# Kernel optimization log

Measured on AMD Instinct MI355X. Metric: run time of the kernel, lower is better.

The kernel has to match this reference:

```python
import jax, jax.numpy as jnp
import numpy as np

B, CIN, COUT, H, W, K, LATENT = 16, 512, 512, 64, 64, 3, 512
SQRT2 = float(np.sqrt(2.0))


def setup_inputs() -> dict:
    key = jax.random.key(0)
    ks = jax.random.split(key, 6)
    return {
        "x": jax.random.normal(ks[0], (B, CIN, H, W), jnp.float32),
        "latent": jax.random.normal(ks[1], (B, LATENT), jnp.float32),
        "noise": jax.random.normal(ks[2], (B, 1, H, W), jnp.float32),
        "affine_weight": jax.random.normal(ks[3], (CIN, LATENT), jnp.float32),
        "affine_bias": jnp.ones((CIN,), jnp.float32),
        "conv_weight": jax.random.normal(ks[4], (COUT, CIN, K, K), jnp.float32),
        "noise_weight": jax.random.normal(ks[5], (), jnp.float32),
        "bias": jnp.zeros((1, COUT, 1, 1), jnp.float32),
    }


def reference(x, latent, noise, affine_weight, affine_bias, conv_weight, noise_weight, bias):
    # NoiseInjection (applied before conv, as in the source)
    x = x + noise_weight * noise

    # AffineNetwork / EqualLinear: w * sqrt(1/in), leaky_relu(.,0.2)*sqrt(2)
    wmul = 1.0 / jnp.sqrt(jnp.float32(affine_weight.shape[1]))
    style = latent @ (affine_weight * wmul).T + affine_bias[None, :]
    style = jax.nn.leaky_relu(style, 0.2) * SQRT2  # [B, Cin]

    # Per-sample modulation (source overwrites the fan-in multiplier; raw weight used)
    w = conv_weight[None] * style[:, None, :, None, None]  # [B, Cout, Cin, kh, kw]
    demod = jax.lax.rsqrt(jnp.sum(w * w, axis=(2, 3, 4), keepdims=True) + 1e-8)
    w = w * demod

    def conv1(xi, wi):  # xi: [Cin,H,W], wi: [Cout,Cin,kh,kw]
        return jax.lax.conv_general_dilated(
            xi[None], wi, (1, 1), "SAME",
            dimension_numbers=("NCHW", "OIHW", "NCHW"))[0]

    out = jax.vmap(conv1)(x, w)  # [B, Cout, H, W]
    return jax.nn.leaky_relu(out + bias, 0.2) * SQRT2
```

## Files before the change

### kernel.cpp

```cpp
#include <hip/hip_runtime.h>

#define SQRT2F 1.41421356237309515f

typedef __attribute__((ext_vector_type(8))) short short8;
typedef __attribute__((ext_vector_type(4))) float floatx4;

static __device__ __forceinline__ unsigned short f2bf(float f) {
    unsigned int u = __float_as_uint(f);
    u += 0x7fffu + ((u >> 16) & 1u);
    return (unsigned short)(u >> 16);
}

static __device__ __forceinline__ void gl_lds16(const void* g, void* l) {
    __builtin_amdgcn_global_load_lds(
        (const __attribute__((address_space(1))) unsigned int*)g,
        (__attribute__((address_space(3))) unsigned int*)l, 16, 0, 0);
}

__global__ void style_kernel(const float* __restrict__ latent,
                             const float* __restrict__ aw,
                             const float* __restrict__ abias,
                             float* __restrict__ style) {
    const int b = blockIdx.x;
    const int t = threadIdx.x;
    __shared__ float lat[512];
    lat[t]       = latent[b * 512 + t];
    lat[t + 256] = latent[b * 512 + t + 256];
    __syncthreads();
    const float wmul = 0.04419417382415922f;
    for (int c = t; c < 512; c += 256) {
        const float* row = aw + (size_t)c * 512;
        float s = 0.f;
        #pragma unroll 8
        for (int k = 0; k < 512; ++k) s += lat[k] * row[k];
        s = s * wmul + abias[c];
        s = (s > 0.f ? s : 0.2f * s) * SQRT2F;
        style[b * 512 + c] = s;
    }
}

__global__ void wprep_kernel(const float* __restrict__ cw,
                             const float* __restrict__ style,
                             unsigned short* __restrict__ wbf,
                             float* __restrict__ demod) {
    const int co = blockIdx.x;
    const int t = threadIdx.x;
    __shared__ float raw[4608];
    __shared__ float sty2[8192];
    __shared__ float r2[512];
    const float* row = cw + (size_t)co * 4608;
    for (int i = t; i < 4608; i += 256) raw[i] = row[i];
    for (int i = t; i < 8192; i += 256) { float v = style[i]; sty2[i] = v * v; }
    __syncthreads();
    for (int cin = t; cin < 512; cin += 256) {
        float s = 0.f;
        #pragma unroll
        for (int tap = 0; tap < 9; ++tap) { float v = raw[cin * 9 + tap]; s += v * v; }
        r2[cin] = s;
    }
    for (int i = t; i < 4608; i += 256) {
        int cin = i / 9, tap = i - cin * 9;
        wbf[(((size_t)(cin >> 5) * 9 + tap) * 512 + co) * 32 + (cin & 31)] = f2bf(raw[i]);
    }
    __syncthreads();
    const int lane = t & 63, wv = t >> 6;
    #pragma unroll
    for (int bb = 0; bb < 4; ++bb) {
        int b = wv * 4 + bb;
        float s = 0.f;
        for (int cin = lane; cin < 512; cin += 64) s += r2[cin] * sty2[b * 512 + cin];
        #pragma unroll
        for (int off = 32; off > 0; off >>= 1) s += __shfl_down(s, off, 64);
        if (lane == 0) demod[b * 512 + co] = rsqrtf(s + 1e-8f);
    }
}

__global__ void xprep_kernel(const float* __restrict__ x,
                             const float* __restrict__ noise,
                             const float* __restrict__ nwp,
                             const float* __restrict__ style,
                             unsigned short* __restrict__ xp) {
    const int h = blockIdx.x, slab = blockIdx.y, b = blockIdx.z;
    const int t = threadIdx.x;
    __shared__ float tile[32][65];
    const int ci4 = t >> 6, w = t & 63;
    const float nv = nwp[0] * noise[(size_t)b * 4096 + h * 64 + w];
    #pragma unroll
    for (int p = 0; p < 8; ++p) {
        int cl = p * 4 + ci4;
        int cin = slab * 32 + cl;
        float v = x[((size_t)(b * 512 + cin)) * 4096 + h * 64 + w];
        tile[cl][w] = (v + nv) * style[b * 512 + cin];
    }
    __syncthreads();
    const int w2 = t >> 2, chunk = t & 3;
    short8 o;
    #pragma unroll
    for (int j = 0; j < 8; ++j) o[j] = (short)f2bf(tile[chunk * 8 + j][w2]);
    *(short8*)(xp + ((size_t)(b * 16 + slab) * 4356 + (h + 1) * 66 + (w2 + 1)) * 32 + chunk * 8) = o;
}

__launch_bounds__(256, 2)
__global__ void conv_kernel(const unsigned short* __restrict__ xp,
                            const unsigned short* __restrict__ wbf,
                            const float* __restrict__ demod,
                            const float* __restrict__ bias,
                            float* __restrict__ out) {
    const int b   = blockIdx.z;
    const int co0 = blockIdx.y * 128;
    const int tr  = blockIdx.x >> 2, tc = blockIdx.x & 3;
    const int h0  = tr * 8, w0 = tc * 16;
    const int tid  = threadIdx.x;
    const int lane = tid & 63, wv = tid >> 6;
    const int wr = wv >> 1, wc = wv & 1;
    const int quad = lane >> 4, l16 = lane & 15;

    __shared__ __align__(16) unsigned short lds_x[2][6144];
    __shared__ __align__(16) unsigned short lds_w[2][12288];

    floatx4 acc[4][4] = {};

    int wso[6];
    #pragma unroll
    for (int it = 0; it < 6; ++it) {
        int co = (it * 64 + (tid >> 2)) & 127;
        int lchunk = (tid & 3) ^ ((co >> 1) & 3);
        wso[it] = (it >> 1) * 32768 + co * 64 + lchunk * 16;
    }
    int xo[3];
    #pragma unroll
    for (int it = 0; it < 3; ++it) {
        int pos = it * 64 + (tid >> 2);
        if (pos > 179) pos = 179;
        int r = pos / 18, c = pos - r * 18;
        int lchunk = (tid & 3) ^ ((pos >> 1) & 3);
        xo[it] = (r * 66 + c) * 64 + lchunk * 16;
    }
    const int wvb = wv * 1024;

    int a_off[4];
    #pragma unroll
    for (int mi = 0; mi < 4; ++mi) {
        int co = wr * 64 + mi * 16 + l16;
        a_off[mi] = co * 32 + (quad ^ ((co >> 1) & 3)) * 8;
    }
    int bo[4][9];
    #pragma unroll
    for (int ni = 0; ni < 4; ++ni)
        #pragma unroll
        for (int kh = 0; kh < 3; ++kh)
            #pragma unroll
            for (int kw = 0; kw < 3; ++kw) {
                int pos = (wc * 4 + ni + kh) * 18 + kw + l16;
                bo[ni][kh * 3 + kw] = pos * 32 + (quad ^ ((pos >> 1) & 3)) * 8;
            }

    const char* xpb = (const char*)xp + ((size_t)b * 16 * 4356 + h0 * 66 + w0) * 64;
    const char* wb0 = (const char*)wbf + (size_t)co0 * 64;

    #pragma unroll
    for (int it = 0; it < 3; ++it)
        gl_lds16(xpb + xo[it], (char*)lds_x[0] + it * 4096 + wvb);
    #pragma unroll
    for (int it = 0; it < 6; ++it)
        gl_lds16(wb0 + wso[it], (char*)lds_w[0] + it * 4096 + wvb);

    for (int s = 0; s < 16; ++s) {
        #pragma unroll
        for (int g = 0; g < 3; ++g) {
            __syncthreads();
            if (g < 2) {
                const char* gw = wb0 + s * 294912 + (g + 1) * 98304;
                char* lw = (char*)lds_w[(s + g + 1) & 1];
                #pragma unroll
                for (int it = 0; it < 6; ++it)
                    gl_lds16(gw + wso[it], lw + it * 4096 + wvb);
            } else if (s < 15) {
                const char* gw = wb0 + (s + 1) * 294912;
                char* lw = (char*)lds_w[(s + 1) & 1];
                #pragma unroll
                for (int it = 0; it < 6; ++it)
                    gl_lds16(gw + wso[it], lw + it * 4096 + wvb);
            }
            if (g == 0 && s < 15) {
                const char* gx = xpb + (size_t)(s + 1) * 278784;
                char* lx = (char*)lds_x[(s + 1) & 1];
                #pragma unroll
                for (int it = 0; it < 3; ++it)
                    gl_lds16(gx + xo[it], lx + it * 4096 + wvb);
            }
            const unsigned short* wbuf = lds_w[(s + g) & 1];
            const unsigned short* xbuf = lds_x[s & 1];
            #pragma unroll
            for (int tl = 0; tl < 3; ++tl) {
                const int tap = g * 3 + tl;
                short8 a[4], bb[4];
                #pragma unroll
                for (int mi = 0; mi < 4; ++mi)
                    a[mi] = *(const short8*)(wbuf + tl * 4096 + a_off[mi]);
                #pragma unroll
                for (int ni = 0; ni < 4; ++ni)
                    bb[ni] = *(const short8*)(xbuf + bo[ni][tap]);
                #pragma unroll
                for (int mi = 0; mi < 4; ++mi)
                    #pragma unroll
                    for (int ni = 0; ni < 4; ++ni)
                        acc[mi][ni] = __builtin_amdgcn_mfma_f32_16x16x32_bf16(
                            a[mi], bb[ni], acc[mi][ni], 0, 0, 0);
            }
        }
    }

    const float* dmb = demod + b * 512;
    #pragma unroll
    for (int mi = 0; mi < 4; ++mi) {
        const int cob = co0 + wr * 64 + mi * 16 + quad * 4;
        float bv[4], dv[4];
        #pragma unroll
        for (int i = 0; i < 4; ++i) { bv[i] = bias[cob + i]; dv[i] = dmb[cob + i]; }
        #pragma unroll
        for (int ni = 0; ni < 4; ++ni) {
            const int gh = h0 + wc * 4 + ni;
            const int gw = w0 + l16;
            #pragma unroll
            for (int i = 0; i < 4; ++i) {
                float v = acc[mi][ni][i] * dv[i] + bv[i];
                v = (v > 0.f ? v : 0.2f * v) * SQRT2F;
                out[(((size_t)b * 512 + cob + i) * 64 + gh) * 64 + gw] = v;
            }
        }
    }
}

extern "C" void kernel_launch(void* const* d_in, const int* in_sizes, int n_in,
                              void* d_out, int out_size, void* d_ws, size_t ws_size,
                              hipStream_t stream) {
    const float* x      = (const float*)d_in[0];
    const float* latent = (const float*)d_in[1];
    const float* noise  = (const float*)d_in[2];
    const float* aw     = (const float*)d_in[3];
    const float* abias  = (const float*)d_in[4];
    const float* cw     = (const float*)d_in[5];
    const float* nwp    = (const float*)d_in[6];
    const float* bias   = (const float*)d_in[7];
    float* out = (float*)d_out;

    float* style         = (float*)d_ws;
    float* demod         = (float*)((char*)d_ws + 32768);
    unsigned short* wbf  = (unsigned short*)((char*)d_ws + 65536);
    unsigned short* xp   = (unsigned short*)((char*)d_ws + 65536 + 4718592);

    hipMemsetAsync(xp, 0, (size_t)16 * 16 * 4356 * 64, stream);
    style_kernel<<<dim3(16), dim3(256), 0, stream>>>(latent, aw, abias, style);
    wprep_kernel<<<dim3(512), dim3(256), 0, stream>>>(cw, style, wbf, demod);
    xprep_kernel<<<dim3(64, 16, 16), dim3(256), 0, stream>>>(x, noise, nwp, style, xp);
    conv_kernel<<<dim3(32, 4, 16), dim3(256), 0, stream>>>(xp, wbf, demod, bias, out);
}
```

Before: 553.9 us.

## Vectorize prep kernels, fold padding zeroing into xprep, reuse conv B fragments

The style, wprep and xprep kernels now use 16-byte vector loads and stores. The separate memset of the padded input buffer is removed, and xprep writes the zero halo itself. The style kernel is split across two blocks per sample. In the conv kernel, input fragments for the 6x3 row/column window are loaded once per slab and reused across kernel rows, which cuts LDS reads, and MFMA sections are wrapped in s_setprio. These changes reduce memory traffic and LDS bandwidth in exchange for more register pressure from holding 18 short8 fragments.

```diff
diff --git a/kernel.cpp b/kernel.cpp
--- a/kernel.cpp
+++ b/kernel.cpp
@@ -23,20 +23,25 @@
                              float* __restrict__ style) {
     const int b = blockIdx.x;
     const int t = threadIdx.x;
+    const int c = blockIdx.y * 256 + t;
     __shared__ float lat[512];
     lat[t]       = latent[b * 512 + t];
     lat[t + 256] = latent[b * 512 + t + 256];
     __syncthreads();
-    const float wmul = 0.04419417382415922f;
-    for (int c = t; c < 512; c += 256) {
-        const float* row = aw + (size_t)c * 512;
-        float s = 0.f;
-        #pragma unroll 8
-        for (int k = 0; k < 512; ++k) s += lat[k] * row[k];
-        s = s * wmul + abias[c];
-        s = (s > 0.f ? s : 0.2f * s) * SQRT2F;
-        style[b * 512 + c] = s;
-    }
+    const float* row = aw + (size_t)c * 512;
+    float s0 = 0.f, s1 = 0.f, s2 = 0.f, s3 = 0.f;
+    #pragma unroll 4
+    for (int k = 0; k < 512; k += 4) {
+        floatx4 r = *(const floatx4*)(row + k);
+        s0 += lat[k]     * r[0];
+        s1 += lat[k + 1] * r[1];
+        s2 += lat[k + 2] * r[2];
+        s3 += lat[k + 3] * r[3];
+    }
+    float s = (s0 + s1) + (s2 + s3);
+    s = s * 0.04419417382415922f + abias[c];
+    s = (s > 0.f ? s : 0.2f * s) * SQRT2F;
+    style[b * 512 + c] = s;
 }
 
 __global__ void wprep_kernel(const float* __restrict__ cw,
@@ -49,8 +54,12 @@
     __shared__ float sty2[8192];
     __shared__ float r2[512];
     const float* row = cw + (size_t)co * 4608;
-    for (int i = t; i < 4608; i += 256) raw[i] = row[i];
-    for (int i = t; i < 8192; i += 256) { float v = style[i]; sty2[i] = v * v; }
+    for (int i = t; i < 1152; i += 256)
+        ((floatx4*)raw)[i] = ((const floatx4*)row)[i];
+    for (int i = t; i < 2048; i += 256) {
+        floatx4 v = ((const floatx4*)style)[i];
+        ((floatx4*)sty2)[i] = v * v;
+    }
     __syncthreads();
     for (int cin = t; cin < 512; cin += 256) {
         float s = 0.f;
@@ -58,9 +67,14 @@
         for (int tap = 0; tap < 9; ++tap) { float v = raw[cin * 9 + tap]; s += v * v; }
         r2[cin] = s;
     }
-    for (int i = t; i < 4608; i += 256) {
-        int cin = i / 9, tap = i - cin * 9;
-        wbf[(((size_t)(cin >> 5) * 9 + tap) * 512 + co) * 32 + (cin & 31)] = f2bf(raw[i]);
+    for (int j = t; j < 576; j += 256) {
+        int st = j >> 2, chunk = j & 3;
+        int slab = st / 9, tap = st - slab * 9;
+        int cb = slab * 32 + chunk * 8;
+        short8 o;
+        #pragma unroll
+        for (int k = 0; k < 8; ++k) o[k] = (short)f2bf(raw[(cb + k) * 9 + tap]);
+        *(short8*)(wbf + ((size_t)st * 512 + co) * 32 + chunk * 8) = o;
     }
     __syncthreads();
     const int lane = t & 63, wv = t >> 6;
@@ -83,21 +97,37 @@
     const int h = blockIdx.x, slab = blockIdx.y, b = blockIdx.z;
     const int t = threadIdx.x;
     __shared__ float tile[32][65];
-    const int ci4 = t >> 6, w = t & 63;
-    const float nv = nwp[0] * noise[(size_t)b * 4096 + h * 64 + w];
-    #pragma unroll
-    for (int p = 0; p < 8; ++p) {
-        int cl = p * 4 + ci4;
+    const float nw = nwp[0];
+    const int w4 = (t & 15) * 4, rh = t >> 4;
+    floatx4 nz = *(const floatx4*)(noise + (size_t)b * 4096 + h * 64 + w4);
+    #pragma unroll
+    for (int p = 0; p < 2; ++p) {
+        int cl = p * 16 + rh;
         int cin = slab * 32 + cl;
-        float v = x[((size_t)(b * 512 + cin)) * 4096 + h * 64 + w];
-        tile[cl][w] = (v + nv) * style[b * 512 + cin];
-    }
-    __syncthreads();
+        floatx4 v = *(const floatx4*)(x + ((size_t)(b * 512 + cin)) * 4096 + h * 64 + w4);
+        float sv = style[b * 512 + cin];
+        #pragma unroll
+        for (int j = 0; j < 4; ++j) tile[cl][w4 + j] = (v[j] + nw * nz[j]) * sv;
+    }
+    __syncthreads();
+    unsigned short* base = xp + ((size_t)(b * 16 + slab) * 4356) * 32;
     const int w2 = t >> 2, chunk = t & 3;
     short8 o;
     #pragma unroll
     for (int j = 0; j < 8; ++j) o[j] = (short)f2bf(tile[chunk * 8 + j][w2]);
-    *(short8*)(xp + ((size_t)(b * 16 + slab) * 4356 + (h + 1) * 66 + (w2 + 1)) * 32 + chunk * 8) = o;
+    *(short8*)(base + ((size_t)(h + 1) * 66 + (w2 + 1)) * 32 + chunk * 8) = o;
+    short8 z = {};
+    if (t < 8) {
+        int col = (t >> 2) * 65;
+        *(short8*)(base + ((size_t)(h + 1) * 66 + col) * 32 + (t & 3) * 8) = z;
+    }
+    if (h == 0) {
+        for (int i = t; i < 264; i += 256)
+            *(short8*)(base + (size_t)(i >> 2) * 32 + (i & 3) * 8) = z;
+    } else if (h == 63) {
+        for (int i = t; i < 264; i += 256)
+            *(short8*)(base + ((size_t)65 * 66 + (i >> 2)) * 32 + (i & 3) * 8) = z;
+    }
 }
 
 __launch_bounds__(256, 2)
@@ -144,16 +174,14 @@
         int co = wr * 64 + mi * 16 + l16;
         a_off[mi] = co * 32 + (quad ^ ((co >> 1) & 3)) * 8;
     }
-    int bo[4][9];
-    #pragma unroll
-    for (int ni = 0; ni < 4; ++ni)
-        #pragma unroll
-        for (int kh = 0; kh < 3; ++kh)
-            #pragma unroll
-            for (int kw = 0; kw < 3; ++kw) {
-                int pos = (wc * 4 + ni + kh) * 18 + kw + l16;
-                bo[ni][kh * 3 + kw] = pos * 32 + (quad ^ ((pos >> 1) & 3)) * 8;
-            }
+    int bo2[6][3];
+    #pragma unroll
+    for (int r = 0; r < 6; ++r)
+        #pragma unroll
+        for (int c = 0; c < 3; ++c) {
+            int pos = (wc * 4 + r) * 18 + c + l16;
+            bo2[r][c] = pos * 32 + (quad ^ ((pos >> 1) & 3)) * 8;
+        }
 
     const char* xpb = (const char*)xp + ((size_t)b * 16 * 4356 + h0 * 66 + w0) * 64;
     const char* wb0 = (const char*)wbf + (size_t)co0 * 64;
@@ -166,6 +194,7 @@
         gl_lds16(wb0 + wso[it], (char*)lds_w[0] + it * 4096 + wvb);
 
     for (int s = 0; s < 16; ++s) {
+        short8 xf[6][3];
         #pragma unroll
         for (int g = 0; g < 3; ++g) {
             __syncthreads();
@@ -191,22 +220,31 @@
             }
             const unsigned short* wbuf = lds_w[(s + g) & 1];
             const unsigned short* xbuf = lds_x[s & 1];
+            if (g == 0) {
+                #pragma unroll
+                for (int r = 0; r < 4; ++r)
+                    #pragma unroll
+                    for (int c = 0; c < 3; ++c)
+                        xf[r][c] = *(const short8*)(xbuf + bo2[r][c]);
+            } else {
+                #pragma unroll
+                for (int c = 0; c < 3; ++c)
+                    xf[g + 3][c] = *(const short8*)(xbuf + bo2[g + 3][c]);
+            }
             #pragma unroll
             for (int tl = 0; tl < 3; ++tl) {
-                const int tap = g * 3 + tl;
-                short8 a[4], bb[4];
+                short8 a[4];
                 #pragma unroll
                 for (int mi = 0; mi < 4; ++mi)
                     a[mi] = *(const short8*)(wbuf + tl * 4096 + a_off[mi]);
-                #pragma unroll
-                for (int ni = 0; ni < 4; ++ni)
-                    bb[ni] = *(const short8*)(xbuf + bo[ni][tap]);
+                __builtin_amdgcn_s_setprio(1);
                 #pragma unroll
                 for (int mi = 0; mi < 4; ++mi)
                     #pragma unroll
                     for (int ni = 0; ni < 4; ++ni)
                         acc[mi][ni] = __builtin_amdgcn_mfma_f32_16x16x32_bf16(
-                            a[mi], bb[ni], acc[mi][ni], 0, 0, 0);
+                            a[mi], xf[ni + g][tl], acc[mi][ni], 0, 0, 0);
+                __builtin_amdgcn_s_setprio(0);
             }
         }
     }
@@ -250,8 +288,7 @@
     unsigned short* wbf  = (unsigned short*)((char*)d_ws + 65536);
     unsigned short* xp   = (unsigned short*)((char*)d_ws + 65536 + 4718592);
 
-    hipMemsetAsync(xp, 0, (size_t)16 * 16 * 4356 * 64, stream);
-    style_kernel<<<dim3(16), dim3(256), 0, stream>>>(latent, aw, abias, style);
+    style_kernel<<<dim3(16, 2), dim3(256), 0, stream>>>(latent, aw, abias, style);
     wprep_kernel<<<dim3(512), dim3(256), 0, stream>>>(cw, style, wbf, demod);
     xprep_kernel<<<dim3(64, 16, 16), dim3(256), 0, stream>>>(x, noise, nwp, style, xp);
     conv_kernel<<<dim3(32, 4, 16), dim3(256), 0, stream>>>(xp, wbf, demod, bias, out);
```

Measured after the change: 501.0 us. 1.11x faster.
